# Kernel tuning notes

Measured on AMD Instinct MI355X. Metric: run time of the kernel, lower is better.

Reference implementation:

```python
import jax, jax.numpy as jnp
import numpy as np

B, S, D, H = 128, 256, 256, 8   # graphs, nodes/graph, dim_h, heads
N = B * S
E = 524288
DH = D // H
BN_EPS = 1e-5

def _bn(v, g, b):
    # BatchNorm1d forward with batch statistics (biased var), eval-dropout model
    m = v.mean(0)
    var = v.var(0)
    return (v - m) * jax.lax.rsqrt(var + BN_EPS) * g + b

def setup_inputs() -> dict:
    key = jax.random.key(0)
    ks = jax.random.split(key, 40)
    x = jax.random.normal(ks[0], (N, D), jnp.float32)
    src = jax.random.randint(ks[1], (E,), 0, N)
    dst = (src // S) * S + jax.random.randint(ks[2], (E,), 0, S)  # intra-graph edges
    edge_index = jnp.stack([src, dst]).astype(jnp.int64)
    def lin(k, i, o):
        return (jax.random.normal(k, (i, o), jnp.float32) / np.float32(np.sqrt(i)))
    inp = {
        'x': x, 'edge_index': edge_index,
        'W_gcn': lin(ks[3], D, D), 'b_gcn': jnp.zeros((D,), jnp.float32),
        'W_gin1': lin(ks[4], D, D), 'b_gin1': jnp.zeros((D,), jnp.float32),
        'W_gin2': lin(ks[5], D, D), 'b_gin2': jnp.zeros((D,), jnp.float32),
        'g_kv': jnp.ones((D,), jnp.float32), 'be_kv': jnp.zeros((D,), jnp.float32),
        'Wq1': lin(ks[6], D, D), 'bq1': jnp.zeros((D,), jnp.float32),
        'Wq2': lin(ks[7], D, D), 'bq2': jnp.zeros((D,), jnp.float32),
        'Wq_a': lin(ks[8], D, D), 'bq_a': jnp.zeros((D,), jnp.float32),
        'Wk_a': lin(ks[9], D, D), 'bk_a': jnp.zeros((D,), jnp.float32),
        'Wv_a': lin(ks[10], D, D), 'bv_a': jnp.zeros((D,), jnp.float32),
        'Wo_a': lin(ks[11], D, D), 'bo_a': jnp.zeros((D,), jnp.float32),
        'g_attn': jnp.ones((D,), jnp.float32), 'be_attn': jnp.zeros((D,), jnp.float32),
        'Wf1': lin(ks[12], D, 2 * D), 'bf1': jnp.zeros((2 * D,), jnp.float32),
        'Wf2': lin(ks[13], 2 * D, D), 'bf2': jnp.zeros((D,), jnp.float32),
        'g2': jnp.ones((D,), jnp.float32), 'be2': jnp.zeros((D,), jnp.float32),
    }
    return inp

def _forward(x, edge_index,
             W_gcn, b_gcn, W_gin1, b_gin1, W_gin2, b_gin2, g_kv, be_kv,
             Wq1, bq1, Wq2, bq2,
             Wq_a, bq_a, Wk_a, bk_a, Wv_a, bv_a, Wo_a, bo_a, g_attn, be_attn,
             Wf1, bf1, Wf2, bf2, g2, be2):
    row, col = edge_index[0], edge_index[1]
    h_in1 = x

    # ---- expert 0: GCNConv (add self loops + symmetric norm) ----
    loops = jnp.arange(N, dtype=row.dtype)
    row2 = jnp.concatenate([row, loops])
    col2 = jnp.concatenate([col, loops])
    deg = jax.ops.segment_sum(jnp.ones_like(row2, jnp.float32), col2, num_segments=N)
    dinv = jnp.where(deg > 0, jax.lax.rsqrt(deg), 0.0)
    norm = dinv[row2] * dinv[col2]                     # [E+N]
    xw = x @ W_gcn                                      # [N, D]
    h_gcn = jax.ops.segment_sum(norm[:, None] * xw[row2], col2, num_segments=N) + b_gcn
    e0 = _bn(h_gcn, g_kv, be_kv)

    # ---- expert 1: GINConv (eps=0, sum aggregation, 2-layer MLP) ----
    agg = jax.ops.segment_sum(x[row], col, num_segments=N)
    h_gin = jax.nn.relu((x + agg) @ W_gin1 + b_gin1) @ W_gin2 + b_gin2
    e1 = _bn(h_gin, g_kv, be_kv)

    # ---- global expert normalization (torch .std -> unbiased) ----
    allo = jnp.concatenate([e0, e1], axis=0)
    gm = allo.mean()
    gs = jnp.std(allo, ddof=1)
    e0 = (e0 - gm) / (gs + 1e-8)
    e1 = (e1 - gm) / (gs + 1e-8)

    # ---- uniform routing & kv residual mix ----
    kv = 0.5 * e0 + 0.5 * e1 + 0.1 * h_in1              # [N, D]

    # ---- dense batching (equal-sized graphs -> pure reshape, full mask) ----
    q_dense = h_in1.reshape(B, S, D)
    kv_dense = kv.reshape(B, S, D)

    # ---- q projection MLP ----
    q_dense = jax.nn.relu(q_dense @ Wq1 + bq1) @ Wq2 + bq2

    # ---- multihead attention (batch_first, no padding) ----
    qh = (q_dense @ Wq_a + bq_a).reshape(B, S, H, DH)
    kh = (kv_dense @ Wk_a + bk_a).reshape(B, S, H, DH)
    vh = (kv_dense @ Wv_a + bv_a).reshape(B, S, H, DH)
    scores = jnp.einsum('bqhd,bkhd->bhqk', qh, kh) / np.float32(np.sqrt(DH))
    attn = jax.nn.softmax(scores, axis=-1)
    o = jnp.einsum('bhqk,bkhd->bqhd', attn, vh).reshape(B, S, D)
    h_attn = (o @ Wo_a + bo_a).reshape(N, D)

    # ---- residual + norm + FFN block ----
    h = _bn(h_in1 + h_attn, g_attn, be_attn)
    h_ff = jax.nn.relu(h @ Wf1 + bf1) @ Wf2 + bf2
    h = _bn(h + h_ff, g2, be2)
    return h

def reference(x, edge_index,
              W_gcn, b_gcn, W_gin1, b_gin1, W_gin2, b_gin2, g_kv, be_kv,
              Wq1, bq1, Wq2, bq2,
              Wq_a, bq_a, Wk_a, bk_a, Wv_a, bv_a, Wo_a, bo_a, g_attn, be_attn,
              Wf1, bf1, Wf2, bf2, g2, be2):
    return _forward(x, edge_index,
                    W_gcn, b_gcn, W_gin1, b_gin1, W_gin2, b_gin2, g_kv, be_kv,
                    Wq1, bq1, Wq2, bq2,
                    Wq_a, bq_a, Wk_a, bk_a, Wv_a, bv_a, Wo_a, bo_a, g_attn, be_attn,
                    Wf1, bf1, Wf2, bf2, g2, be2)
```

## Files before the change

### kernel.cpp

```cpp
#include <hip/hip_runtime.h>
#include <hip/hip_bf16.h>

typedef __hip_bfloat16 bf16;
typedef __attribute__((ext_vector_type(8))) short short8;
typedef __attribute__((ext_vector_type(4))) short short4v;
typedef __attribute__((ext_vector_type(4))) float f32x4;
typedef __attribute__((ext_vector_type(4))) int i32x4;

#define N_ 32768
#define D_ 256
#define S_ 256
#define B_ 128
#define E_ 524288

static __device__ __forceinline__ f32x4 mfma16(short8 a, short8 b, f32x4 c) {
  return __builtin_amdgcn_mfma_f32_16x16x32_bf16(a, b, c, 0, 0, 0);
}
static __device__ __forceinline__ f32x4 fzero4() {
  f32x4 z; z[0] = 0.f; z[1] = 0.f; z[2] = 0.f; z[3] = 0.f; return z;
}
static __device__ __forceinline__ float bits2f(short s) {
  unsigned u = ((unsigned)(unsigned short)s) << 16;
  return __builtin_bit_cast(float, u);
}
static __device__ __forceinline__ short f2bits(float f) {
  bf16 b = __float2bfloat16(f);
  return __builtin_bit_cast(short, b);
}
static __device__ __forceinline__ float tof(float x) { return x; }
static __device__ __forceinline__ float tof(bf16 x) { return __bfloat162float(x); }

#define GLOAD_LDS16(G, L) __builtin_amdgcn_global_load_lds( \
    (const __attribute__((address_space(1))) void*)(G),     \
    (__attribute__((address_space(3))) void*)(L), 16, 0, 0)

template<int F>
__global__ __launch_bounds__(256)
void gemm_bt(const bf16* __restrict__ A, const bf16* __restrict__ Bt,
             const float* __restrict__ bias, const float* __restrict__ biasB,
             const void* __restrict__ resid,
             float* __restrict__ Cf, bf16* __restrict__ Cb,
             float* __restrict__ Sp, float* __restrict__ SSp,
             int M, int Nc, int K, long bsA, long bsB, long bsC)
{
  __shared__ __align__(16) bf16 lA[128 * 32];
  __shared__ __align__(16) bf16 lB[128 * 32];
  __shared__ float sS[2][128], sSS[2][128];
  const int z = blockIdx.z;
  const bf16* Ab = A + (long)z * bsA;
  const bf16* Bb = Bt + (long)z * bsB;
  const int m0 = blockIdx.x * 128, n0 = blockIdx.y * 128;
  const int tid = threadIdx.x;
  const int lane = tid & 63;
  const int w = tid >> 6, wr = w >> 1, wc = w & 1;
  const int g = lane >> 4, r = lane & 15, ko = g * 8;
  const int srow = lane >> 2, skw = (lane & 3) * 8;

  f32x4 acc[4][4];
  for (int i = 0; i < 4; i++) for (int j = 0; j < 4; j++) acc[i][j] = fzero4();

  for (int k0 = 0; k0 < K; k0 += 32) {
    __syncthreads();
    for (int i = 0; i < 2; i++) {
      const int c = w * 2 + i;
      GLOAD_LDS16(Ab + (long)(m0 + c * 16 + srow) * K + k0 + skw, lA + c * 512);
      GLOAD_LDS16(Bb + (long)(n0 + c * 16 + srow) * K + k0 + skw, lB + c * 512);
    }
    __syncthreads();
    short8 af[4], bfv[4];
    for (int mi = 0; mi < 4; mi++)
      af[mi] = *(const short8*)&lA[(wr * 64 + mi * 16 + r) * 32 + ko];
    for (int ni = 0; ni < 4; ni++)
      bfv[ni] = *(const short8*)&lB[(wc * 64 + ni * 16 + r) * 32 + ko];
    for (int mi = 0; mi < 4; mi++)
      for (int ni = 0; ni < 4; ni++)
        acc[mi][ni] = mfma16(af[mi], bfv[ni], acc[mi][ni]);
  }

  float cs[4] = {0, 0, 0, 0}, css[4] = {0, 0, 0, 0};
  for (int mi = 0; mi < 4; mi++) for (int ni = 0; ni < 4; ni++) {
    const int row = m0 + wr * 64 + mi * 16 + g * 4;
    const int col = n0 + wc * 64 + ni * 16 + r;
    float bv = 0.0f;
    if (F & 2) {
      if ((F & 128) && col >= 256) bv = biasB[col - 256];
      else bv = bias[col];
    }
    for (int j = 0; j < 4; j++) {
      long idx = (long)(row + j) * Nc + col;
      float v = acc[mi][ni][j] + bv;
      if (F & 4)  v += ((const float*)resid)[(long)z * bsC + idx];
      if (F & 64) v += bits2f(((const short*)resid)[(long)z * bsC + idx]);
      if (F & 1)  v = fmaxf(v, 0.0f);
      if (F & 32) { cs[ni] += v; css[ni] += v * v; }
      if (F & 8)  Cf[(long)z * bsC + idx] = v;
      if (F & 16) Cb[(long)z * bsC + idx] = __float2bfloat16(v);
    }
  }
  if (F & 32) {
    for (int ni = 0; ni < 4; ni++) {
      cs[ni]  += __shfl_xor(cs[ni], 16);  cs[ni]  += __shfl_xor(cs[ni], 32);
      css[ni] += __shfl_xor(css[ni], 16); css[ni] += __shfl_xor(css[ni], 32);
    }
    if (lane < 16) {
      for (int ni = 0; ni < 4; ni++) {
        sS[wr][wc * 64 + ni * 16 + lane]  = cs[ni];
        sSS[wr][wc * 64 + ni * 16 + lane] = css[ni];
      }
    }
    __syncthreads();
    if (tid < 128) {
      atomicAdd(&Sp[n0 + tid],  sS[0][tid] + sS[1][tid]);
      atomicAdd(&SSp[n0 + tid], sSS[0][tid] + sSS[1][tid]);
    }
  }
}

template<int STAGES, bool STATS>
__global__ __launch_bounds__(512)
void mlp_fused(const bf16* __restrict__ A,
               const bf16* __restrict__ B1, const float* __restrict__ b1,
               const bf16* __restrict__ B2, const float* __restrict__ b2,
               const bf16* __restrict__ B3, const float* __restrict__ b3,
               bf16* __restrict__ C, float* __restrict__ Sp, float* __restrict__ SSp)
{
  __shared__ __align__(16) bf16 lA[64 * 32];
  __shared__ __align__(16) bf16 lB[256 * 32];
  __shared__ __align__(16) bf16 lC[64 * 256];
  char* lCc = (char*)lC;
  const int tid = threadIdx.x;
  const int lane = tid & 63;
  const int w = tid >> 6;
  const int mh = w >> 2, nq = w & 3;
  const int g = lane >> 4, r = lane & 15, ko = g * 8;
  const int m0 = blockIdx.x * 64;

  f32x4 acc[2][4];
  for (int i = 0; i < 2; i++) for (int j = 0; j < 4; j++) acc[i][j] = fzero4();

  for (int k0 = 0; k0 < 256; k0 += 32) {
    __syncthreads();
    if (tid < 256)
      GLOAD_LDS16(A + (long)(m0 + (tid >> 2)) * 256 + k0 + (tid & 3) * 8,
                  lA + w * 512);
    GLOAD_LDS16(B1 + (long)(tid >> 2) * 256 + k0 + (tid & 3) * 8,
                lB + w * 512);
    GLOAD_LDS16(B1 + (long)((tid + 512) >> 2) * 256 + k0 + ((tid + 512) & 3) * 8,
                lB + w * 512 + 4096);
    __syncthreads();
    short8 af[2], bfv[4];
    for (int mi = 0; mi < 2; mi++)
      af[mi] = *(const short8*)&lA[(mh * 32 + mi * 16 + r) * 32 + ko];
    for (int ni = 0; ni < 4; ni++)
      bfv[ni] = *(const short8*)&lB[(nq * 64 + ni * 16 + r) * 32 + ko];
    for (int mi = 0; mi < 2; mi++)
      for (int ni = 0; ni < 4; ni++)
        acc[mi][ni] = mfma16(af[mi], bfv[ni], acc[mi][ni]);
  }
  for (int mi = 0; mi < 2; mi++) for (int ni = 0; ni < 4; ni++) {
    const int col = nq * 64 + ni * 16 + r;
    const float bv = b1[col];
    for (int j = 0; j < 4; j++) {
      const int row = mh * 32 + mi * 16 + g * 4 + j;
      float v = fmaxf(acc[mi][ni][j] + bv, 0.0f);
      *(short*)(lCc + ((row * 512 + col * 2) ^ ((row & 7) << 4))) = f2bits(v);
    }
  }
  __syncthreads();

  const bf16* Bs = B2;
  for (int s = 1; s < STAGES; s++) {
    for (int i = 0; i < 2; i++) for (int j = 0; j < 4; j++) acc[i][j] = fzero4();
    for (int k0 = 0; k0 < 256; k0 += 32) {
      __syncthreads();
      GLOAD_LDS16(Bs + (long)(tid >> 2) * 256 + k0 + (tid & 3) * 8,
                  lB + w * 512);
      GLOAD_LDS16(Bs + (long)((tid + 512) >> 2) * 256 + k0 + ((tid + 512) & 3) * 8,
                  lB + w * 512 + 4096);
      __syncthreads();
      short8 af[2], bfv[4];
      for (int mi = 0; mi < 2; mi++) {
        const int row = mh * 32 + mi * 16 + r;
        af[mi] = *(const short8*)(lCc +
                  ((row * 512 + (k0 + ko) * 2) ^ ((row & 7) << 4)));
      }
      for (int ni = 0; ni < 4; ni++)
        bfv[ni] = *(const short8*)&lB[(nq * 64 + ni * 16 + r) * 32 + ko];
      for (int mi = 0; mi < 2; mi++)
        for (int ni = 0; ni < 4; ni++)
          acc[mi][ni] = mfma16(af[mi], bfv[ni], acc[mi][ni]);
    }
    if (s < STAGES - 1) {
      __syncthreads();
      for (int mi = 0; mi < 2; mi++) for (int ni = 0; ni < 4; ni++) {
        const int col = nq * 64 + ni * 16 + r;
        const float bv = b2[col];
        for (int j = 0; j < 4; j++) {
          const int row = mh * 32 + mi * 16 + g * 4 + j;
          float v = acc[mi][ni][j] + bv;
          *(short*)(lCc + ((row * 512 + col * 2) ^ ((row & 7) << 4))) = f2bits(v);
        }
      }
      __syncthreads();
      Bs = B3;
    }
  }

  const float* bf_ = (STAGES == 3) ? b3 : b2;
  float cs[4] = {0, 0, 0, 0}, css[4] = {0, 0, 0, 0};
  for (int mi = 0; mi < 2; mi++) for (int ni = 0; ni < 4; ni++) {
    const int col = nq * 64 + ni * 16 + r;
    const float bv = bf_[col];
    for (int j = 0; j < 4; j++) {
      const int row = mh * 32 + mi * 16 + g * 4 + j;
      float v = acc[mi][ni][j] + bv;
      if (STATS) { cs[ni] += v; css[ni] += v * v; }
      C[(long)(m0 + row) * 256 + col] = __float2bfloat16(v);
    }
  }
  if (STATS) {
    for (int ni = 0; ni < 4; ni++) {
      cs[ni]  += __shfl_xor(cs[ni], 16);  cs[ni]  += __shfl_xor(cs[ni], 32);
      css[ni] += __shfl_xor(css[ni], 16); css[ni] += __shfl_xor(css[ni], 32);
    }
    __syncthreads();
    float* sS = (float*)lC;
    if (lane < 16) {
      for (int ni = 0; ni < 4; ni++) {
        sS[mh * 256 + nq * 64 + ni * 16 + lane] = cs[ni];
        sS[512 + mh * 256 + nq * 64 + ni * 16 + lane] = css[ni];
      }
    }
    __syncthreads();
    if (tid < 256) {
      atomicAdd(&Sp[tid],  sS[tid] + sS[256 + tid]);
      atomicAdd(&SSp[tid], sS[512 + tid] + sS[768 + tid]);
    }
  }
}

__global__ __launch_bounds__(256, 2)
void attn_k(const bf16* __restrict__ qh, const bf16* __restrict__ kh,
            const bf16* __restrict__ vh, bf16* __restrict__ ob, int ks)
{
  const int h = blockIdx.x, b = blockIdx.y;
  const int tid = threadIdx.x, lane = tid & 63, w = tid >> 6;
  const int g = lane >> 4, r = lane & 15, ko = g * 8;
  __shared__ __align__(16) bf16 lK[256 * 32];
  __shared__ __align__(16) bf16 lV[32 * 256];
  char* lKc = (char*)lK;
  char* lVc = (char*)lV;

  for (int i = 0; i < 4; i++) {
    int c = tid + i * 256;
    int row = c >> 2, p4 = c & 3;
    short8 v = *(const short8*)(kh + (long)(b * 256 + row) * ks + h * 32 + p4 * 8);
    *(short8*)(lKc + ((row * 64 + p4 * 16) ^ ((row & 7) << 4))) = v;
  }
  for (int i = 0; i < 4; i++) {
    int c = tid + i * 256;
    int s = c >> 2, part = c & 3;
    short8 v = *(const short8*)(vh + (long)(b * 256 + s) * ks + h * 32 + part * 8);
    for (int j = 0; j < 8; j++) {
      int dh = part * 8 + j;
      int sw = ((dh & 7) ^ ((dh >> 3) << 1)) & 7;
      *(short*)(lVc + ((dh * 512 + s * 2) ^ (sw << 4))) = v[j];
    }
  }
  __syncthreads();

  const float scale = 0.17677669529663687f;
  const int idx0 = (((lane >> 4) & 1) * 32 + r) * 4;
  const int idx1 = idx0 + 64;
  const bool selhi = lane >= 32;

  for (int mc = 0; mc < 4; mc++) {
    const long qbase = (long)b * 256 + w * 64 + mc * 16;
    short8 qf = *(const short8*)(qh + (qbase + r) * 256 + h * 32 + ko);
    f32x4 sc[16];
    __builtin_amdgcn_s_setprio(1);
    #pragma unroll
    for (int nc = 0; nc < 16; nc++) {
      int row = nc * 16 + r;
      short8 kf = *(const short8*)(lKc + ((row * 64 + g * 16) ^ ((r & 7) << 4)));
      sc[nc] = mfma16(kf, qf, fzero4());
    }
    __builtin_amdgcn_s_setprio(0);
    f32x4 m4 = sc[0];
    #pragma unroll
    for (int nc = 1; nc < 16; nc++)
      for (int j = 0; j < 4; j++) m4[j] = fmaxf(m4[j], sc[nc][j]);
    float mx = fmaxf(fmaxf(m4[0], m4[1]), fmaxf(m4[2], m4[3]));
    mx = fmaxf(mx, __shfl_xor(mx, 16));
    mx = fmaxf(mx, __shfl_xor(mx, 32));
    f32x4 s4 = fzero4();
    #pragma unroll
    for (int nc = 0; nc < 16; nc++)
      for (int j = 0; j < 4; j++) {
        float p = __expf((sc[nc][j] - mx) * scale);
        sc[nc][j] = p; s4[j] += p;
      }
    float sum = s4[0] + s4[1] + s4[2] + s4[3];
    sum += __shfl_xor(sum, 16);
    sum += __shfl_xor(sum, 32);
    const float invs = 1.0f / sum;
    f32x4 oa[2]; oa[0] = fzero4(); oa[1] = fzero4();
    __builtin_amdgcn_s_setprio(1);
    #pragma unroll
    for (int kc = 0; kc < 8; kc++) {
      int pkA0, pkA1, pkB0, pkB1;
      {
        const f32x4 pa = sc[2 * kc], pb = sc[2 * kc + 1];
        unsigned a0 = (unsigned short)f2bits(pa[0] * invs);
        unsigned a1 = (unsigned short)f2bits(pa[1] * invs);
        unsigned a2 = (unsigned short)f2bits(pa[2] * invs);
        unsigned a3 = (unsigned short)f2bits(pa[3] * invs);
        unsigned b0 = (unsigned short)f2bits(pb[0] * invs);
        unsigned b1 = (unsigned short)f2bits(pb[1] * invs);
        unsigned b2 = (unsigned short)f2bits(pb[2] * invs);
        unsigned b3 = (unsigned short)f2bits(pb[3] * invs);
        pkA0 = (int)((a1 << 16) | a0);
        pkA1 = (int)((a3 << 16) | a2);
        pkB0 = (int)((b1 << 16) | b0);
        pkB1 = (int)((b3 << 16) | b2);
      }
      int A0 = __builtin_amdgcn_ds_bpermute(idx0, pkA0);
      int A1 = __builtin_amdgcn_ds_bpermute(idx0, pkA1);
      int B0 = __builtin_amdgcn_ds_bpermute(idx0, pkB0);
      int B1 = __builtin_amdgcn_ds_bpermute(idx0, pkB1);
      int C0 = __builtin_amdgcn_ds_bpermute(idx1, pkA0);
      int C1 = __builtin_amdgcn_ds_bpermute(idx1, pkA1);
      int D0 = __builtin_amdgcn_ds_bpermute(idx1, pkB0);
      int D1 = __builtin_amdgcn_ds_bpermute(idx1, pkB1);
      i32x4 av;
      av[0] = selhi ? B0 : A0;
      av[1] = selhi ? B1 : A1;
      av[2] = selhi ? D0 : C0;
      av[3] = selhi ? D1 : C1;
      short8 af = __builtin_bit_cast(short8, av);
      #pragma unroll
      for (int n = 0; n < 2; n++) {
        int dh = n * 16 + r;
        int sw = ((dh & 7) ^ ((dh >> 3) << 1)) & 7;
        short8 bv = *(const short8*)(lVc + ((dh * 512 + kc * 64 + g * 16) ^ (sw << 4)));
        oa[n] = mfma16(af, bv, oa[n]);
      }
    }
    __builtin_amdgcn_s_setprio(0);
    #pragma unroll
    for (int n = 0; n < 2; n++)
      for (int j = 0; j < 4; j++)
        ob[(qbase + g * 4 + j) * 256 + h * 32 + n * 16 + r] =
          __float2bfloat16(oa[n][j]);
  }
}

template<typename TIN>
__global__ __launch_bounds__(256)
void transpose_cast_k(const TIN* __restrict__ in, bf16* __restrict__ out,
                      int in_rs, int out_rs, long zhi, long out_zs)
{
  __shared__ float tile[32][33];
  const int z = blockIdx.z;
  const long ioff = (long)z * zhi;
  const long ooff = (long)z * out_zs;
  const int tx = threadIdx.x, ty = threadIdx.y;
  const int c = blockIdx.x * 32 + tx;
  const int rb = blockIdx.y * 32;
  for (int i = 0; i < 4; i++)
    tile[ty + i * 8][tx] = tof(in[ioff + (long)(rb + ty + i * 8) * in_rs + c]);
  __syncthreads();
  const int oc = rb + tx;
  const int orb = blockIdx.x * 32;
  for (int i = 0; i < 4; i++)
    out[ooff + (long)(orb + ty + i * 8) * out_rs + oc] =
      __float2bfloat16(tile[tx][ty + i * 8]);
}

__global__ __launch_bounds__(256)
void w9t_k(const float* w0, const float* w1, const float* w2, const float* w3,
           const float* w4, const float* w5, const float* w6, const float* w7,
           const float* w8, bf16* __restrict__ out)
{
  __shared__ float tile[32][33];
  const float* srcs[9] = {w0, w1, w2, w3, w4, w5, w6, w7, w8};
  const int wi = blockIdx.z;
  const float* in = srcs[wi];
  bf16* o = out + (long)wi * 65536;
  const int tx = threadIdx.x, ty = threadIdx.y;
  const int c = blockIdx.x * 32 + tx;
  const int rb = blockIdx.y * 32;
  for (int i = 0; i < 4; i++)
    tile[ty + i * 8][tx] = in[(rb + ty + i * 8) * 256 + c];
  __syncthreads();
  const int oc = rb + tx;
  const int orb = blockIdx.x * 32;
  for (int i = 0; i < 4; i++)
    o[(orb + ty + i * 8) * 256 + oc] = __float2bfloat16(tile[tx][ty + i * 8]);
}

__global__ __launch_bounds__(256)
void cast4_k(const float* __restrict__ in, bf16* __restrict__ out)
{
  long i = ((long)blockIdx.x * 256 + threadIdx.x) * 4;
  float4 v = *(const float4*)(in + i);
  short4v o;
  o[0] = f2bits(v.x); o[1] = f2bits(v.y); o[2] = f2bits(v.z); o[3] = f2bits(v.w);
  *(short4v*)(out + i) = o;
}

__global__ __launch_bounds__(256)
void edge_cnt_k(const int* __restrict__ ei, unsigned* __restrict__ cnt)
{
  int e = blockIdx.x * 256 + threadIdx.x;
  int src = ei[e], dst = ei[E_ + e];
  long idx = ((long)(src >> 8) * 256 + (dst & 255)) * 256 + (src & 255);
  atomicAdd(&cnt[idx >> 1], 1u << ((idx & 1) * 16));
}

__global__ __launch_bounds__(256)
void deg_k(const unsigned* __restrict__ cnt, float* __restrict__ dinv)
{
  int rid = blockIdx.x * 16 + (threadIdx.x >> 4);
  int l16 = threadIdx.x & 15;
  const uint4* rp = (const uint4*)(cnt + (long)rid * 128);
  unsigned s = 0;
  for (int i = 0; i < 2; i++) {
    uint4 v = rp[l16 + i * 16];
    s += (v.x & 0xFFFF) + (v.x >> 16) + (v.y & 0xFFFF) + (v.y >> 16)
       + (v.z & 0xFFFF) + (v.z >> 16) + (v.w & 0xFFFF) + (v.w >> 16);
  }
  s += __shfl_xor(s, 1); s += __shfl_xor(s, 2);
  s += __shfl_xor(s, 4); s += __shfl_xor(s, 8);
  if (l16 == 0) dinv[rid] = rsqrtf((float)s + 1.0f);
}

__global__ __launch_bounds__(256)
void adj_derive_k(const unsigned* __restrict__ cnt, const float* __restrict__ dinv,
                  bf16* __restrict__ gin, bf16* __restrict__ gcn)
{
  long i = ((long)blockIdx.x * 256 + threadIdx.x) * 4;
  uint2 cp = *(const uint2*)(cnt + (i >> 1));
  float cv[4] = {(float)(cp.x & 0xFFFF), (float)(cp.x >> 16),
                 (float)(cp.y & 0xFFFF), (float)(cp.y >> 16)};
  long row = i >> 8;
  int g = (int)(row >> 8), dst = (int)(row & 255);
  int src0 = (int)(i & 255);
  float dd = dinv[row];
  const float* ds = dinv + (long)g * 256 + src0;
  short4v oi, oc;
  for (int j = 0; j < 4; j++) {
    float gv = cv[j] * dd * ds[j];
    if (src0 + j == dst) gv += dd * dd;
    oi[j] = f2bits(cv[j]);
    oc[j] = f2bits(gv);
  }
  *(short4v*)(gin + i) = oi;
  *(short4v*)(gcn + i) = oc;
}

__global__ __launch_bounds__(256)
void expert_stats_k(const float* __restrict__ S0, const float* __restrict__ SS0,
                    const float* __restrict__ S1, const float* __restrict__ SS1,
                    const float* __restrict__ gkv, const float* __restrict__ bkv,
                    float* __restrict__ kA, float* __restrict__ kB,
                    float* __restrict__ kC)
{
  const int d = threadIdx.x;
  const float invN = 1.0f / 32768.0f;
  float m0 = S0[d] * invN, v0 = SS0[d] * invN - m0 * m0;
  float a0 = gkv[d] * rsqrtf(v0 + 1e-5f), c0 = bkv[d] - m0 * a0;
  float m1 = S1[d] * invN, v1 = SS1[d] * invN - m1 * m1;
  float a1 = gkv[d] * rsqrtf(v1 + 1e-5f), c1 = bkv[d] - m1 * a1;
  float gsum = a0 * S0[d] + 32768.0f * c0 + a1 * S1[d] + 32768.0f * c1;
  float gss  = a0 * a0 * SS0[d] + 2.0f * a0 * c0 * S0[d] + 32768.0f * c0 * c0
             + a1 * a1 * SS1[d] + 2.0f * a1 * c1 * S1[d] + 32768.0f * c1 * c1;
  __shared__ float r1[256], r2[256];
  r1[d] = gsum; r2[d] = gss;
  __syncthreads();
  for (int s = 128; s > 0; s >>= 1) {
    if (d < s) { r1[d] += r1[d + s]; r2[d] += r2[d + s]; }
    __syncthreads();
  }
  const float cntall = 16777216.0f;
  float tg = r1[0], tss = r2[0];
  float gm = tg / cntall;
  float var = (tss - tg * tg / cntall) / (cntall - 1.0f);
  float gs = sqrtf(fmaxf(var, 0.f)) + 1e-8f;
  kA[d] = 0.5f * a0 / gs;
  kB[d] = 0.5f * a1 / gs;
  kC[d] = 0.5f * (c0 + c1 - 2.0f * gm) / gs;
}

__global__ __launch_bounds__(256)
void kv_mix_k(const bf16* __restrict__ hgcn, const bf16* __restrict__ hgin,
              const bf16* __restrict__ xb, const float* __restrict__ kA,
              const float* __restrict__ kB, const float* __restrict__ kC,
              bf16* __restrict__ kv)
{
  long i = ((long)blockIdx.x * 256 + threadIdx.x) * 8;
  int d0 = (int)(i & 255);
  short8 a = *(const short8*)(hgcn + i);
  short8 b = *(const short8*)(hgin + i);
  short8 c = *(const short8*)(xb + i);
  short8 o;
  for (int j = 0; j < 8; j++) {
    int d = d0 + j;
    float v = kA[d] * bits2f(a[j]) + kB[d] * bits2f(b[j]) + kC[d] + 0.1f * bits2f(c[j]);
    o[j] = f2bits(v);
  }
  *(short8*)(kv + i) = o;
}

template<int MODE>
__global__ __launch_bounds__(256)
void bn_apply_k(const bf16* __restrict__ in, const float* __restrict__ S,
                const float* __restrict__ SSq, const float* __restrict__ gg,
                const float* __restrict__ bb, float* __restrict__ outf,
                bf16* __restrict__ outb)
{
  long i = ((long)blockIdx.x * 256 + threadIdx.x) * 8;
  int d0 = (int)(i & 255);
  short8 v = *(const short8*)(in + i);
  const float invN = 1.0f / 32768.0f;
  float4 o0, o1; short8 o8;
  for (int j = 0; j < 8; j++) {
    int d = d0 + j;
    float m = S[d] * invN;
    float var = SSq[d] * invN - m * m;
    float a = gg[d] * rsqrtf(var + 1e-5f);
    float c = bb[d] - m * a;
    float o = a * bits2f(v[j]) + c;
    if (MODE & 1) { if (j < 4) (&o0.x)[j] = o; else (&o1.x)[j - 4] = o; }
    if (MODE & 2) o8[j] = f2bits(o);
  }
  if (MODE & 1) { *(float4*)(outf + i) = o0; *(float4*)(outf + i + 4) = o1; }
  if (MODE & 2) *(short8*)(outb + i) = o8;
}

static constexpr size_t OFF_S0 = 0, OFF_SS0 = 1024, OFF_S1 = 2048, OFF_SS1 = 3072;
static constexpr size_t OFF_S2 = 4096, OFF_SS2 = 5120, OFF_S3 = 6144, OFF_SS3 = 7168;
static constexpr size_t OFF_KA = 8192, OFF_KB = 9216, OFF_KC = 10240;
static constexpr size_t OFF_CNT = 16384;
static constexpr size_t CNT_BYTES = (size_t)B_ * S_ * S_ * 2;
static constexpr size_t ZERO_BYTES = OFF_CNT + CNT_BYTES;
static constexpr size_t OFF_DINV = ZERO_BYTES;
static constexpr size_t OFF_W = OFF_DINV + 131072;
static constexpr size_t NDB2 = (size_t)N_ * D_ * 2;
static constexpr size_t OFF_ADJGINB = OFF_W + 1703936;
static constexpr size_t OFF_ADJGCNB = OFF_ADJGINB + NDB2;
static constexpr size_t OFF_XB   = OFF_ADJGCNB + NDB2;
static constexpr size_t OFF_XT   = OFF_XB + NDB2;
static constexpr size_t OFF_AGG  = OFF_XT + NDB2;
static constexpr size_t OFF_GIN  = OFF_AGG + NDB2;
static constexpr size_t OFF_KV   = OFF_GIN + NDB2;
static constexpr size_t OFF_HGCN = OFF_KV + NDB2;
static constexpr size_t OFF_HGIN = OFF_HGCN + NDB2;

extern "C" void kernel_launch(void* const* d_in, const int* in_sizes, int n_in,
                              void* d_out, int out_size, void* d_ws, size_t ws_size,
                              hipStream_t stream)
{
  (void)in_sizes; (void)n_in; (void)out_size; (void)ws_size;
  const float* x      = (const float*)d_in[0];
  const int*   ei     = (const int*)d_in[1];
  const float* W_gcn  = (const float*)d_in[2];
  const float* b_gcn  = (const float*)d_in[3];
  const float* W_gin1 = (const float*)d_in[4];
  const float* b_gin1 = (const float*)d_in[5];
  const float* W_gin2 = (const float*)d_in[6];
  const float* b_gin2 = (const float*)d_in[7];
  const float* g_kv   = (const float*)d_in[8];
  const float* be_kv  = (const float*)d_in[9];
  const float* Wq1    = (const float*)d_in[10];
  const float* bq1    = (const float*)d_in[11];
  const float* Wq2    = (const float*)d_in[12];
  const float* bq2    = (const float*)d_in[13];
  const float* Wq_a   = (const float*)d_in[14];
  const float* bq_a   = (const float*)d_in[15];
  const float* Wk_a   = (const float*)d_in[16];
  const float* bk_a   = (const float*)d_in[17];
  const float* Wv_a   = (const float*)d_in[18];
  const float* bv_a   = (const float*)d_in[19];
  const float* Wo_a   = (const float*)d_in[20];
  const float* bo_a   = (const float*)d_in[21];
  const float* g_attn = (const float*)d_in[22];
  const float* be_attn= (const float*)d_in[23];
  const float* Wf1    = (const float*)d_in[24];
  const float* bf1    = (const float*)d_in[25];
  const float* Wf2    = (const float*)d_in[26];
  const float* bf2    = (const float*)d_in[27];
  const float* g2     = (const float*)d_in[28];
  const float* be2    = (const float*)d_in[29];

  char* ws = (char*)d_ws;
  float* S0  = (float*)(ws + OFF_S0);  float* SS0 = (float*)(ws + OFF_SS0);
  float* S1  = (float*)(ws + OFF_S1);  float* SS1 = (float*)(ws + OFF_SS1);
  float* S2  = (float*)(ws + OFF_S2);  float* SS2 = (float*)(ws + OFF_SS2);
  float* S3  = (float*)(ws + OFF_S3);  float* SS3 = (float*)(ws + OFF_SS3);
  float* kA  = (float*)(ws + OFF_KA);  float* kB  = (float*)(ws + OFF_KB);
  float* kC  = (float*)(ws + OFF_KC);
  unsigned* cntA = (unsigned*)(ws + OFF_CNT);
  float* dinv = (float*)(ws + OFF_DINV);
  bf16* wT = (bf16*)(ws + OFF_W);
  bf16 *WgcnT = wT,            *Wgin1T = wT + 65536,  *Wgin2T = wT + 131072;
  bf16 *Wq1T  = wT + 196608,   *Wq2T   = wT + 262144, *WqaT   = wT + 327680;
  bf16 *WkaT  = wT + 393216,   *WvaT   = wT + 458752, *WoaT   = wT + 524288;
  bf16 *Wf1T  = wT + 589824,   *Wf2T   = wT + 720896;
  (void)WvaT;
  bf16* adjGINb = (bf16*)(ws + OFF_ADJGINB);
  bf16* adjGCNb = (bf16*)(ws + OFF_ADJGCNB);
  bf16* xb    = (bf16*)(ws + OFF_XB);
  bf16* xT    = (bf16*)(ws + OFF_XT);
  bf16* aggb  = (bf16*)(ws + OFF_AGG);
  bf16* gin_in= (bf16*)(ws + OFF_GIN);
  bf16* kv_bf = (bf16*)(ws + OFF_KV);
  bf16* hgcnb = (bf16*)(ws + OFF_HGCN);
  bf16* hginb = (bf16*)(ws + OFF_HGIN);
  bf16* qhb    = adjGINb;
  bf16* khvb   = aggb;
  bf16* ob     = hginb;
  bf16* tbufb  = (bf16*)(ws + OFF_CNT);
  bf16* hb     = xb;
  bf16* f1b    = adjGINb;
  bf16* t2b    = (bf16*)(ws + OFF_CNT);
  float* outp  = (float*)d_out;

  hipMemsetAsync(d_ws, 0, ZERO_BYTES, stream);

  dim3 tb(32, 8);
  w9t_k<<<dim3(8, 8, 9), tb, 0, stream>>>(W_gcn, W_gin1, W_gin2, Wq1, Wq2,
                                          Wq_a, Wk_a, Wv_a, Wo_a, wT);
  transpose_cast_k<float><<<dim3(16, 8, 1), tb, 0, stream>>>(Wf1, Wf1T, 512, 256, 0, 0);
  transpose_cast_k<float><<<dim3(8, 16, 1), tb, 0, stream>>>(Wf2, Wf2T, 256, 512, 0, 0);
  cast4_k<<<8192, 256, 0, stream>>>(x, xb);
  transpose_cast_k<float><<<dim3(8, 8, 128), tb, 0, stream>>>(x, xT, 256, 256, 65536, 65536);
  edge_cnt_k<<<2048, 256, 0, stream>>>(ei, cntA);
  deg_k<<<2048, 256, 0, stream>>>(cntA, dinv);
  adj_derive_k<<<8192, 256, 0, stream>>>(cntA, dinv, adjGINb, adjGCNb);
  gemm_bt<16><<<dim3(2, 2, 128), 256, 0, stream>>>(adjGCNb, xT, nullptr, nullptr,
      nullptr, nullptr, aggb, nullptr, nullptr, 256, 256, 256, 65536, 65536, 65536);
  gemm_bt<80><<<dim3(2, 2, 128), 256, 0, stream>>>(adjGINb, xT, nullptr, nullptr,
      xb, nullptr, gin_in, nullptr, nullptr, 256, 256, 256, 65536, 65536, 65536);
  gemm_bt<50><<<dim3(256, 2, 1), 256, 0, stream>>>(aggb, WgcnT, b_gcn, nullptr,
      nullptr, nullptr, hgcnb, S0, SS0, N_, 256, 256, 0, 0, 0);
  mlp_fused<2, true><<<512, 512, 0, stream>>>(gin_in, Wgin1T, b_gin1,
      Wgin2T, b_gin2, nullptr, nullptr, hginb, S1, SS1);
  expert_stats_k<<<1, 256, 0, stream>>>(S0, SS0, S1, SS1, g_kv, be_kv, kA, kB, kC);
  kv_mix_k<<<4096, 256, 0, stream>>>(hgcnb, hginb, xb, kA, kB, kC, kv_bf);
  mlp_fused<3, false><<<512, 512, 0, stream>>>(xb, Wq1T, bq1,
      Wq2T, bq2, WqaT, bq_a, qhb, nullptr, nullptr);
  gemm_bt<146><<<dim3(256, 4, 1), 256, 0, stream>>>(kv_bf, WkaT, bk_a, bv_a,
      nullptr, nullptr, khvb, nullptr, nullptr, N_, 512, 256, 0, 0, 0);
  attn_k<<<dim3(8, 128), 256, 0, stream>>>(qhb, khvb, khvb + 256, ob, 512);
  gemm_bt<114><<<dim3(256, 2, 1), 256, 0, stream>>>(ob, WoaT, bo_a, nullptr,
      xb, nullptr, tbufb, S2, SS2, N_, 256, 256, 0, 0, 0);
  bn_apply_k<2><<<4096, 256, 0, stream>>>(tbufb, S2, SS2, g_attn, be_attn, nullptr, hb);
  gemm_bt<19><<<dim3(256, 4, 1), 256, 0, stream>>>(hb, Wf1T, bf1, nullptr,
      nullptr, nullptr, f1b, nullptr, nullptr, N_, 512, 256, 0, 0, 0);
  gemm_bt<114><<<dim3(256, 2, 1), 256, 0, stream>>>(f1b, Wf2T, bf2, nullptr,
      hb, nullptr, t2b, S3, SS3, N_, 256, 512, 0, 0, 0);
  bn_apply_k<1><<<4096, 256, 0, stream>>>(t2b, S3, SS3, g2, be2, outp, nullptr);
}
```

Measured before the change: 331.1 us.

## Split attention over query halves, pack edge counts to bytes, fuse x prep

The attention kernel now runs twice as many blocks, each handling half the query rows. It builds the V transpose in shared memory with packed 32-bit writes and computes the softmax exponent as one fma plus exp2. Edge-count bins shrink from 16 to 8 bits, which halves the zeroed count buffer and the traffic in the degree and adjacency kernels. The bf16 cast and the transpose of x are merged into one kernel so x is read once. The risks are count overflow if any edge is repeated more than 255 times, and K/V being loaded twice per head because two blocks now share it.

After: 319.5 us. -3.5%, faster.

```diff
diff --git a/kernel.cpp b/kernel.cpp
--- a/kernel.cpp
+++ b/kernel.cpp
@@ -243,7 +243,7 @@
 void attn_k(const bf16* __restrict__ qh, const bf16* __restrict__ kh,
             const bf16* __restrict__ vh, bf16* __restrict__ ob, int ks)
 {
-  const int h = blockIdx.x, b = blockIdx.y;
+  const int h = blockIdx.x, qhf = blockIdx.y, b = blockIdx.z;
   const int tid = threadIdx.x, lane = tid & 63, w = tid >> 6;
   const int g = lane >> 4, r = lane & 15, ko = g * 8;
   __shared__ __align__(16) bf16 lK[256 * 32];
@@ -257,25 +257,30 @@
     short8 v = *(const short8*)(kh + (long)(b * 256 + row) * ks + h * 32 + p4 * 8);
     *(short8*)(lKc + ((row * 64 + p4 * 16) ^ ((row & 7) << 4))) = v;
   }
-  for (int i = 0; i < 4; i++) {
+  for (int i = 0; i < 2; i++) {
     int c = tid + i * 256;
-    int s = c >> 2, part = c & 3;
-    short8 v = *(const short8*)(vh + (long)(b * 256 + s) * ks + h * 32 + part * 8);
+    int sp = c >> 2, part = c & 3;
+    const bf16* vp = vh + (long)(b * 256 + 2 * sp) * ks + h * 32 + part * 8;
+    short8 va = *(const short8*)(vp);
+    short8 vb = *(const short8*)(vp + ks);
+    #pragma unroll
     for (int j = 0; j < 8; j++) {
       int dh = part * 8 + j;
       int sw = ((dh & 7) ^ ((dh >> 3) << 1)) & 7;
-      *(short*)(lVc + ((dh * 512 + s * 2) ^ (sw << 4))) = v[j];
+      unsigned wrd = ((unsigned)(unsigned short)vb[j] << 16) |
+                     (unsigned)(unsigned short)va[j];
+      *(unsigned*)(lVc + ((dh * 512 + sp * 4) ^ (sw << 4))) = wrd;
     }
   }
   __syncthreads();
 
-  const float scale = 0.17677669529663687f;
+  const float c1 = 0.17677669529663687f * 1.4426950408889634f;
   const int idx0 = (((lane >> 4) & 1) * 32 + r) * 4;
   const int idx1 = idx0 + 64;
   const bool selhi = lane >= 32;
 
-  for (int mc = 0; mc < 4; mc++) {
-    const long qbase = (long)b * 256 + w * 64 + mc * 16;
+  for (int mc = 0; mc < 2; mc++) {
+    const long qbase = (long)b * 256 + qhf * 128 + w * 32 + mc * 16;
     short8 qf = *(const short8*)(qh + (qbase + r) * 256 + h * 32 + ko);
     f32x4 sc[16];
     __builtin_amdgcn_s_setprio(1);
@@ -293,11 +298,12 @@
     float mx = fmaxf(fmaxf(m4[0], m4[1]), fmaxf(m4[2], m4[3]));
     mx = fmaxf(mx, __shfl_xor(mx, 16));
     mx = fmaxf(mx, __shfl_xor(mx, 32));
+    const float mxc = mx * c1;
     f32x4 s4 = fzero4();
     #pragma unroll
     for (int nc = 0; nc < 16; nc++)
       for (int j = 0; j < 4; j++) {
-        float p = __expf((sc[nc][j] - mx) * scale);
+        float p = exp2f(fmaf(sc[nc][j], c1, -mxc));
         sc[nc][j] = p; s4[j] += p;
       }
     float sum = s4[0] + s4[1] + s4[2] + s4[3];
@@ -378,6 +384,29 @@
 }
 
 __global__ __launch_bounds__(256)
+void xprep_k(const float* __restrict__ x, bf16* __restrict__ xb,
+             bf16* __restrict__ xT)
+{
+  __shared__ float tile[32][33];
+  const int z = blockIdx.z;
+  const long ioff = (long)z * 65536;
+  const int tx = threadIdx.x, ty = threadIdx.y;
+  const int c = blockIdx.x * 32 + tx;
+  const int rb = blockIdx.y * 32;
+  for (int i = 0; i < 4; i++) {
+    float v = x[ioff + (long)(rb + ty + i * 8) * 256 + c];
+    tile[ty + i * 8][tx] = v;
+    xb[ioff + (long)(rb + ty + i * 8) * 256 + c] = __float2bfloat16(v);
+  }
+  __syncthreads();
+  const int oc = rb + tx;
+  const int orb = blockIdx.x * 32;
+  for (int i = 0; i < 4; i++)
+    xT[ioff + (long)(orb + ty + i * 8) * 256 + oc] =
+      __float2bfloat16(tile[tx][ty + i * 8]);
+}
+
+__global__ __launch_bounds__(256)
 void w9t_k(const float* w0, const float* w1, const float* w2, const float* w3,
            const float* w4, const float* w5, const float* w6, const float* w7,
            const float* w8, bf16* __restrict__ out)
@@ -400,22 +429,12 @@
 }
 
 __global__ __launch_bounds__(256)
-void cast4_k(const float* __restrict__ in, bf16* __restrict__ out)
-{
-  long i = ((long)blockIdx.x * 256 + threadIdx.x) * 4;
-  float4 v = *(const float4*)(in + i);
-  short4v o;
-  o[0] = f2bits(v.x); o[1] = f2bits(v.y); o[2] = f2bits(v.z); o[3] = f2bits(v.w);
-  *(short4v*)(out + i) = o;
-}
-
-__global__ __launch_bounds__(256)
 void edge_cnt_k(const int* __restrict__ ei, unsigned* __restrict__ cnt)
 {
   int e = blockIdx.x * 256 + threadIdx.x;
   int src = ei[e], dst = ei[E_ + e];
   long idx = ((long)(src >> 8) * 256 + (dst & 255)) * 256 + (src & 255);
-  atomicAdd(&cnt[idx >> 1], 1u << ((idx & 1) * 16));
+  atomicAdd(&cnt[idx >> 2], 1u << ((idx & 3) * 8));
 }
 
 __global__ __launch_bounds__(256)
@@ -423,13 +442,12 @@
 {
   int rid = blockIdx.x * 16 + (threadIdx.x >> 4);
   int l16 = threadIdx.x & 15;
-  const uint4* rp = (const uint4*)(cnt + (long)rid * 128);
+  uint4 v = ((const uint4*)(cnt + (long)rid * 64))[l16];
   unsigned s = 0;
-  for (int i = 0; i < 2; i++) {
-    uint4 v = rp[l16 + i * 16];
-    s += (v.x & 0xFFFF) + (v.x >> 16) + (v.y & 0xFFFF) + (v.y >> 16)
-       + (v.z & 0xFFFF) + (v.z >> 16) + (v.w & 0xFFFF) + (v.w >> 16);
-  }
+  s += (v.x & 0xFF) + ((v.x >> 8) & 0xFF) + ((v.x >> 16) & 0xFF) + (v.x >> 24);
+  s += (v.y & 0xFF) + ((v.y >> 8) & 0xFF) + ((v.y >> 16) & 0xFF) + (v.y >> 24);
+  s += (v.z & 0xFF) + ((v.z >> 8) & 0xFF) + ((v.z >> 16) & 0xFF) + (v.z >> 24);
+  s += (v.w & 0xFF) + ((v.w >> 8) & 0xFF) + ((v.w >> 16) & 0xFF) + (v.w >> 24);
   s += __shfl_xor(s, 1); s += __shfl_xor(s, 2);
   s += __shfl_xor(s, 4); s += __shfl_xor(s, 8);
   if (l16 == 0) dinv[rid] = rsqrtf((float)s + 1.0f);
@@ -439,10 +457,11 @@
 void adj_derive_k(const unsigned* __restrict__ cnt, const float* __restrict__ dinv,
                   bf16* __restrict__ gin, bf16* __restrict__ gcn)
 {
-  long i = ((long)blockIdx.x * 256 + threadIdx.x) * 4;
-  uint2 cp = *(const uint2*)(cnt + (i >> 1));
-  float cv[4] = {(float)(cp.x & 0xFFFF), (float)(cp.x >> 16),
-                 (float)(cp.y & 0xFFFF), (float)(cp.y >> 16)};
+  long wi = (long)blockIdx.x * 256 + threadIdx.x;
+  unsigned cw = cnt[wi];
+  long i = wi * 4;
+  float cv[4] = {(float)(cw & 0xFF), (float)((cw >> 8) & 0xFF),
+                 (float)((cw >> 16) & 0xFF), (float)(cw >> 24)};
   long row = i >> 8;
   int g = (int)(row >> 8), dst = (int)(row & 255);
   int src0 = (int)(i & 255);
@@ -542,9 +561,9 @@
 static constexpr size_t OFF_S2 = 4096, OFF_SS2 = 5120, OFF_S3 = 6144, OFF_SS3 = 7168;
 static constexpr size_t OFF_KA = 8192, OFF_KB = 9216, OFF_KC = 10240;
 static constexpr size_t OFF_CNT = 16384;
-static constexpr size_t CNT_BYTES = (size_t)B_ * S_ * S_ * 2;
+static constexpr size_t CNT_BYTES = (size_t)B_ * S_ * S_;
 static constexpr size_t ZERO_BYTES = OFF_CNT + CNT_BYTES;
-static constexpr size_t OFF_DINV = ZERO_BYTES;
+static constexpr size_t OFF_DINV = OFF_CNT + (size_t)B_ * S_ * S_ * 2;
 static constexpr size_t OFF_W = OFF_DINV + 131072;
 static constexpr size_t NDB2 = (size_t)N_ * D_ * 2;
 static constexpr size_t OFF_ADJGINB = OFF_W + 1703936;
@@ -633,8 +652,7 @@
                                           Wq_a, Wk_a, Wv_a, Wo_a, wT);
   transpose_cast_k<float><<<dim3(16, 8, 1), tb, 0, stream>>>(Wf1, Wf1T, 512, 256, 0, 0);
   transpose_cast_k<float><<<dim3(8, 16, 1), tb, 0, stream>>>(Wf2, Wf2T, 256, 512, 0, 0);
-  cast4_k<<<8192, 256, 0, stream>>>(x, xb);
-  transpose_cast_k<float><<<dim3(8, 8, 128), tb, 0, stream>>>(x, xT, 256, 256, 65536, 65536);
+  xprep_k<<<dim3(8, 8, 128), tb, 0, stream>>>(x, xb, xT);
   edge_cnt_k<<<2048, 256, 0, stream>>>(ei, cntA);
   deg_k<<<2048, 256, 0, stream>>>(cntA, dinv);
   adj_derive_k<<<8192, 256, 0, stream>>>(cntA, dinv, adjGINb, adjGCNb);
@@ -652,7 +670,7 @@
       Wq2T, bq2, WqaT, bq_a, qhb, nullptr, nullptr);
   gemm_bt<146><<<dim3(256, 4, 1), 256, 0, stream>>>(kv_bf, WkaT, bk_a, bv_a,
       nullptr, nullptr, khvb, nullptr, nullptr, N_, 512, 256, 0, 0, 0);
-  attn_k<<<dim3(8, 128), 256, 0, stream>>>(qhb, khvb, khvb + 256, ob, 512);
+  attn_k<<<dim3(8, 2, 128), 256, 0, stream>>>(qhb, khvb, khvb + 256, ob, 512);
   gemm_bt<114><<<dim3(256, 2, 1), 256, 0, stream>>>(ob, WoaT, bo_a, nullptr,
       xb, nullptr, tbufb, S2, SS2, N_, 256, 256, 0, 0, 0);
   bn_apply_k<2><<<4096, 256, 0, stream>>>(tbufb, S2, SS2, g_attn, be_attn, nullptr, hb);
```
